# Performance work log

Hardware: AMD Instinct MI355X
Metric: run time of the kernel (lower is better)

## Reference

```python
import jax, jax.numpy as jnp
import numpy as np
from jax import lax

IMG_H, IMG_W = 800.0, 800.0
REG_WEIGHTS = (10.0, 10.0, 5.0, 5.0)
SCORE_THRESH = 0.05
NMS_THRESH = 0.5
NUM_DETECTIONS = 100
MIN_SIZE = 1.0
BBOX_XFORM_CLIP = float(np.log(1000.0 / 16.0))


def setup_inputs() -> dict:
    key = jax.random.key(0)
    k1, k2, k3, k4 = jax.random.split(key, 4)
    N, C = 1000, 81
    class_logit = jax.random.normal(k1, (N, C), dtype=jnp.float32) * 2.0
    box_regression = jax.random.normal(k2, (N, C * 4), dtype=jnp.float32)
    # proposals: valid (x1,y1,x2,y2) boxes inside the 800x800 image
    ctr = jax.random.uniform(k3, (N, 2), dtype=jnp.float32) * 800.0
    wh = jax.random.uniform(k4, (N, 2), dtype=jnp.float32) * 200.0 + 8.0
    x1y1 = jnp.clip(ctr - 0.5 * wh, 0.0, 800.0)
    x2y2 = jnp.clip(ctr + 0.5 * wh, 0.0, 800.0)
    proposal = jnp.concatenate([x1y1, x2y2], axis=1)
    return dict(class_logit=class_logit, box_regression=box_regression, proposal=proposal)


def decode_boxes(deltas, boxes):
    # deltas: [..., 4] (dx,dy,dw,dh); boxes: [..., 4] (x1,y1,x2,y2)
    wx, wy, ww, wh = REG_WEIGHTS
    widths = boxes[..., 2] - boxes[..., 0]
    heights = boxes[..., 3] - boxes[..., 1]
    ctr_x = boxes[..., 0] + 0.5 * widths
    ctr_y = boxes[..., 1] + 0.5 * heights
    dx = deltas[..., 0] / wx
    dy = deltas[..., 1] / wy
    dw = jnp.minimum(deltas[..., 2] / ww, BBOX_XFORM_CLIP)
    dh = jnp.minimum(deltas[..., 3] / wh, BBOX_XFORM_CLIP)
    pcx = dx * widths + ctr_x
    pcy = dy * heights + ctr_y
    pw = jnp.exp(dw) * widths
    ph = jnp.exp(dh) * heights
    return jnp.stack([pcx - 0.5 * pw, pcy - 0.5 * ph, pcx + 0.5 * pw, pcy + 0.5 * ph], axis=-1)


def pairwise_iou(b):
    # b: [N, 4] -> [N, N]
    area = (b[:, 2] - b[:, 0]) * (b[:, 3] - b[:, 1])
    lt = jnp.maximum(b[:, None, :2], b[None, :, :2])
    rb = jnp.minimum(b[:, None, 2:], b[None, :, 2:])
    wh = jnp.clip(rb - lt, 0.0)
    inter = wh[..., 0] * wh[..., 1]
    return inter / (area[:, None] + area[None, :] - inter + 1e-9)


def nms_one_class(boxes, scores):
    # boxes: [N, 4]; scores: [N] with invalid entries masked to -1.
    # Exact greedy NMS: sort by score desc, suppress IoU > NMS_THRESH.
    N = boxes.shape[0]
    order = jnp.argsort(-scores)
    b = boxes[order]
    s = scores[order]
    iou = pairwise_iou(b)
    valid = s > -0.5

    def body(carry, xs):
        keep, i = carry
        row, v = xs
        suppressed = jnp.any(keep & (row > NMS_THRESH))
        keep = keep.at[i].set(v & jnp.logical_not(suppressed))
        return (keep, i + 1), None

    (keep, _), _ = lax.scan(body, (jnp.zeros((N,), bool), jnp.int32(0)), (iou, valid))
    s_kept = jnp.where(keep, s, -1.0)
    top_s, top_i = lax.top_k(s_kept, NUM_DETECTIONS)  # kept are already score-sorted
    out_valid = top_s > -0.5
    out_boxes = jnp.where(out_valid[:, None], b[top_i], 0.0)
    out_scores = jnp.where(out_valid, top_s, 0.0)
    return out_boxes, out_scores, out_valid


def reference(class_logit, box_regression, proposal):
    N, C = class_logit.shape
    pred_score = jax.nn.softmax(class_logit, axis=-1)           # [N, C]
    deltas = box_regression.reshape(N, C, 4)
    boxes = decode_boxes(deltas[:, 1:, :], proposal[:, None, :])  # [N, C-1, 4]
    # clip to image (process_box)
    boxes = jnp.stack([
        jnp.clip(boxes[..., 0], 0.0, IMG_W),
        jnp.clip(boxes[..., 1], 0.0, IMG_H),
        jnp.clip(boxes[..., 2], 0.0, IMG_W),
        jnp.clip(boxes[..., 3], 0.0, IMG_H),
    ], axis=-1)
    w = boxes[..., 2] - boxes[..., 0]
    h = boxes[..., 3] - boxes[..., 1]
    score_fg = pred_score[:, 1:]                                 # [N, C-1]
    valid = (score_fg >= SCORE_THRESH) & (w >= MIN_SIZE) & (h >= MIN_SIZE)
    scores_m = jnp.where(valid, score_fg, -1.0)
    boxes_c = jnp.transpose(boxes, (1, 0, 2))                    # [C-1, N, 4]
    scores_c = scores_m.T                                        # [C-1, N]
    out_boxes, out_scores, out_valid = jax.vmap(nms_one_class)(boxes_c, scores_c)
    labels = jnp.broadcast_to(jnp.arange(1, C, dtype=jnp.int32)[:, None], out_scores.shape)
    labels = jnp.where(out_valid, labels, 0)
    # padded per-class detections: boxes [C-1, D, 4], scores/labels/valid [C-1, D]
    return out_boxes, out_scores, labels, out_valid
```

## Files before the change

### kernel.cpp

```cpp
#include <hip/hip_runtime.h>
#include <math.h>

#define N_PROP   1000
#define C_ALL    81
#define N_FG     80
#define TOPK     100
#define CAP      1024
#define IMG_WH   800.0f
#define SCORE_TH 0.05f
#define NMS_TH   0.5f
#define MIN_SZ   1.0f
#define BBOX_CLIP 4.135166556742356f

#define BLK      512

typedef unsigned long long u64;

__global__ __launch_bounds__(BLK) void roihead_kernel(
    const float* __restrict__ logits,
    const float* __restrict__ boxreg,
    const float* __restrict__ prop,
    float* __restrict__ out)
{
    __shared__ float2 s_stats[N_PROP];
    __shared__ u64   s_key[CAP];
    __shared__ float cx1[CAP], cy1[CAP], cx2[CAP], cy2[CAP], car[CAP];
    __shared__ u64   s_skey[CAP];
    __shared__ float sx1[CAP], sy1[CAP], sx2[CAP], sy2[CAP], sar[CAP];
    __shared__ u64   s_mask[256 * 4];
    __shared__ u64   s_keep[4];
    __shared__ unsigned char s_rem[CAP];
    __shared__ int   s_cnt, s_emit;

    const int c   = blockIdx.x;
    const int tid = threadIdx.x;
    const int col = c + 1;

    const int OFF_SCORES = N_FG * TOPK * 4;
    const int OFF_LABELS = OFF_SCORES + N_FG * TOPK;
    const int OFF_VALID  = OFF_LABELS + N_FG * TOPK;

    if (tid < 175) {
        float4 z = make_float4(0.f, 0.f, 0.f, 0.f);
        if (tid < 100)      ((float4*)(out + c * TOPK * 4))[tid] = z;
        else if (tid < 125) ((float4*)(out + OFF_SCORES + c * TOPK))[tid - 100] = z;
        else if (tid < 150) ((float4*)(out + OFF_LABELS + c * TOPK))[tid - 125] = z;
        else                ((float4*)(out + OFF_VALID  + c * TOPK))[tid - 150] = z;
    }
    if (tid == 0) { s_cnt = 0; s_emit = 0; }

    for (int n = tid; n < N_PROP; n += BLK) {
        const float* row = logits + n * C_ALL;
        float rv[C_ALL];
        #pragma unroll
        for (int j = 0; j < C_ALL; ++j) rv[j] = row[j];
        float m = rv[0];
        #pragma unroll
        for (int j = 1; j < C_ALL; ++j) m = fmaxf(m, rv[j]);
        float s = 0.0f;
        #pragma unroll
        for (int j = 0; j < C_ALL; ++j) s += expf(rv[j] - m);
        s_stats[n] = make_float2(m, s);
    }
    __syncthreads();

    for (int n = tid; n < N_PROP; n += BLK) {
        float2 ms = s_stats[n];
        float score = expf(logits[n * C_ALL + col] - ms.x) / ms.y;

        float4 p = *(const float4*)(prop + n * 4);
        float w  = p.z - p.x;
        float h  = p.w - p.y;
        float pcx0 = p.x + 0.5f * w;
        float pcy0 = p.y + 0.5f * h;

        float4 d = *(const float4*)(boxreg + n * (C_ALL * 4) + col * 4);
        float dx = d.x / 10.0f;
        float dy = d.y / 10.0f;
        float dw = fminf(d.z / 5.0f, BBOX_CLIP);
        float dh = fminf(d.w / 5.0f, BBOX_CLIP);

        float pcx = dx * w + pcx0;
        float pcy = dy * h + pcy0;
        float pw  = expf(dw) * w;
        float ph  = expf(dh) * h;

        float x1 = fminf(fmaxf(pcx - 0.5f * pw, 0.0f), IMG_WH);
        float y1 = fminf(fmaxf(pcy - 0.5f * ph, 0.0f), IMG_WH);
        float x2 = fminf(fmaxf(pcx + 0.5f * pw, 0.0f), IMG_WH);
        float y2 = fminf(fmaxf(pcy + 0.5f * ph, 0.0f), IMG_WH);

        float bw = x2 - x1;
        float bh = y2 - y1;
        if (score >= SCORE_TH && bw >= MIN_SZ && bh >= MIN_SZ) {
            int slot = atomicAdd(&s_cnt, 1);
            unsigned int fb = __float_as_uint(score);
            s_key[slot] = ((u64)fb << 20) | ((u64)(1023 - n) << 10) | (u64)slot;
            cx1[slot] = x1; cy1[slot] = y1; cx2[slot] = x2; cy2[slot] = y2;
            car[slot] = bw * bh;
        }
    }
    __syncthreads();

    const int V = s_cnt;
    if (V == 0) return;

    for (int t = tid; t < V; t += BLK) {
        u64 myk = s_key[t];
        int rank = 0;
        #pragma unroll 4
        for (int j = 0; j < V; ++j) rank += (s_key[j] > myk) ? 1 : 0;
        s_skey[rank] = myk;
        sx1[rank] = cx1[t]; sy1[rank] = cy1[t];
        sx2[rank] = cx2[t]; sy2[rank] = cy2[t];
        sar[rank] = car[t];
    }
    __syncthreads();

    if (V <= 64) {
        if (tid < 64) {
            const int lane = tid;
            bool act = lane < V;
            float bx1 = 0.f, by1 = 0.f, bx2 = 0.f, by2 = 0.f, bar = 0.f;
            if (act) {
                bx1 = sx1[lane]; by1 = sy1[lane];
                bx2 = sx2[lane]; by2 = sy2[lane];
                bar = sar[lane];
            }
            u64 myrow = 0;
            for (int i = 0; i < V; ++i) {
                float ix1 = __shfl(bx1, i, 64);
                float iy1 = __shfl(by1, i, 64);
                float ix2 = __shfl(bx2, i, 64);
                float iy2 = __shfl(by2, i, 64);
                float iar = __shfl(bar, i, 64);
                float lx = fmaxf(ix1, bx1);
                float ly = fmaxf(iy1, by1);
                float rx = fminf(ix2, bx2);
                float ry = fminf(iy2, by2);
                float iw = fmaxf(rx - lx, 0.0f);
                float ih = fmaxf(ry - ly, 0.0f);
                float inter = iw * ih;
                float iou = inter / (iar + bar - inter + 1e-9f);
                u64 bal = __ballot(act && (iou > NMS_TH));
                if (lane == i) {
                    u64 upper = (i == 63) ? 0ull : ~((1ull << (i + 1)) - 1ull);
                    myrow = bal & upper;
                }
            }
            u64 S = 0, K = 0;
            for (int i = 0; i < V; ++i) {
                if (!((S >> i) & 1ull)) {
                    K |= 1ull << i;
                    S |= __shfl(myrow, i, 64);
                }
            }
            if (act && ((K >> lane) & 1ull)) {
                int rank = __popcll(K & ((1ull << lane) - 1ull));
                float score = __uint_as_float((unsigned int)(s_skey[lane] >> 20));
                out[(c * TOPK + rank) * 4 + 0] = bx1;
                out[(c * TOPK + rank) * 4 + 1] = by1;
                out[(c * TOPK + rank) * 4 + 2] = bx2;
                out[(c * TOPK + rank) * 4 + 3] = by2;
                out[OFF_SCORES + c * TOPK + rank] = score;
                out[OFF_LABELS + c * TOPK + rank] = (float)col;
                out[OFF_VALID  + c * TOPK + rank] = 1.0f;
            }
        }
    } else if (V <= 256) {
        for (int i = tid; i < V; i += BLK) {
            float x1i = sx1[i], y1i = sy1[i], x2i = sx2[i], y2i = sy2[i];
            float ai  = sar[i];
            for (int w = 0; w < 4; ++w) {
                u64 mrow = 0;
                int j0 = w << 6;
                int j1 = min(V, j0 + 64);
                for (int j = max(j0, i + 1); j < j1; ++j) {
                    float lx = fmaxf(x1i, sx1[j]);
                    float ly = fmaxf(y1i, sy1[j]);
                    float rx = fminf(x2i, sx2[j]);
                    float ry = fminf(y2i, sy2[j]);
                    float iw = fmaxf(rx - lx, 0.0f);
                    float ih = fmaxf(ry - ly, 0.0f);
                    float inter = iw * ih;
                    float iou = inter / (ai + sar[j] - inter + 1e-9f);
                    if (iou > NMS_TH) mrow |= 1ull << (j - j0);
                }
                s_mask[(i << 2) + w] = mrow;
            }
        }
        __syncthreads();

        if (tid == 0) {
            u64 r0 = 0, r1 = 0, r2 = 0, r3 = 0;
            u64 k0 = 0, k1 = 0, k2 = 0, k3 = 0;
            int kept = 0;
            u64 p0 = s_mask[0], p1 = s_mask[1], p2 = s_mask[2], p3 = s_mask[3];
            u64 q0 = 0, q1 = 0, q2 = 0, q3 = 0;
            if (V > 1) {
                const u64* nr = &s_mask[4];
                q0 = nr[0]; q1 = nr[1]; q2 = nr[2]; q3 = nr[3];
            }
            for (int i = 0; i < V; ++i) {
                u64 t0 = 0, t1 = 0, t2 = 0, t3 = 0;
                if (i + 2 < V) {
                    const u64* nr = &s_mask[(i + 2) << 2];
                    t0 = nr[0]; t1 = nr[1]; t2 = nr[2]; t3 = nr[3];
                }
                int w = i >> 6;
                u64 bit = 1ull << (i & 63);
                u64 rw = (w == 0) ? r0 : (w == 1) ? r1 : (w == 2) ? r2 : r3;
                if (!(rw & bit)) {
                    if (w == 0) k0 |= bit; else if (w == 1) k1 |= bit;
                    else if (w == 2) k2 |= bit; else k3 |= bit;
                    if (++kept >= TOPK) break;
                    r0 |= p0; r1 |= p1; r2 |= p2; r3 |= p3;
                }
                p0 = q0; p1 = q1; p2 = q2; p3 = q3;
                q0 = t0; q1 = t1; q2 = t2; q3 = t3;
            }
            s_keep[0] = k0; s_keep[1] = k1; s_keep[2] = k2; s_keep[3] = k3;
        }
        __syncthreads();

        u64 kw0 = s_keep[0], kw1 = s_keep[1], kw2 = s_keep[2], kw3 = s_keep[3];
        for (int t = tid; t < V; t += BLK) {
            int w = t >> 6;
            u64 kw = (w == 0) ? kw0 : (w == 1) ? kw1 : (w == 2) ? kw2 : kw3;
            if (!((kw >> (t & 63)) & 1ull)) continue;
            int rank = 0;
            if (w > 0) rank += __popcll(kw0);
            if (w > 1) rank += __popcll(kw1);
            if (w > 2) rank += __popcll(kw2);
            rank += __popcll(kw & ((1ull << (t & 63)) - 1ull));
            if (rank < TOPK) {
                float score = __uint_as_float((unsigned int)(s_skey[t] >> 20));
                out[(c * TOPK + rank) * 4 + 0] = sx1[t];
                out[(c * TOPK + rank) * 4 + 1] = sy1[t];
                out[(c * TOPK + rank) * 4 + 2] = sx2[t];
                out[(c * TOPK + rank) * 4 + 3] = sy2[t];
                out[OFF_SCORES + c * TOPK + rank] = score;
                out[OFF_LABELS + c * TOPK + rank] = (float)col;
                out[OFF_VALID  + c * TOPK + rank] = 1.0f;
            }
        }
    } else {
        for (int t = tid; t < V; t += BLK) s_rem[t] = 0;
        __syncthreads();
        for (int i = 0; i < V; ++i) {
            if (s_rem[i]) continue;
            if (tid == 0) {
                int k = s_emit;
                if (k < TOPK) {
                    float score = __uint_as_float((unsigned int)(s_skey[i] >> 20));
                    out[(c * TOPK + k) * 4 + 0] = sx1[i];
                    out[(c * TOPK + k) * 4 + 1] = sy1[i];
                    out[(c * TOPK + k) * 4 + 2] = sx2[i];
                    out[(c * TOPK + k) * 4 + 3] = sy2[i];
                    out[OFF_SCORES + c * TOPK + k] = score;
                    out[OFF_LABELS + c * TOPK + k] = (float)col;
                    out[OFF_VALID  + c * TOPK + k] = 1.0f;
                }
                s_emit = k + 1;
            }
            float x1i = sx1[i], y1i = sy1[i], x2i = sx2[i], y2i = sy2[i];
            float ai  = sar[i];
            for (int jj = i + 1 + tid; jj < V; jj += BLK) {
                if (s_rem[jj]) continue;
                float lx = fmaxf(x1i, sx1[jj]);
                float ly = fmaxf(y1i, sy1[jj]);
                float rx = fminf(x2i, sx2[jj]);
                float ry = fminf(y2i, sy2[jj]);
                float iw = fmaxf(rx - lx, 0.0f);
                float ih = fmaxf(ry - ly, 0.0f);
                float inter = iw * ih;
                float iou = inter / (ai + sar[jj] - inter + 1e-9f);
                if (iou > NMS_TH) s_rem[jj] = 1;
            }
            __syncthreads();
            if (s_emit >= TOPK) break;
        }
    }
}

extern "C" void kernel_launch(void* const* d_in, const int* in_sizes, int n_in,
                              void* d_out, int out_size, void* d_ws, size_t ws_size,
                              hipStream_t stream) {
    const float* class_logit = (const float*)d_in[0];
    const float* box_reg     = (const float*)d_in[1];
    const float* proposal    = (const float*)d_in[2];
    float* out = (float*)d_out;

    roihead_kernel<<<N_FG, BLK, 0, stream>>>(class_logit, box_reg, proposal,
                                             out);
}
```

Before: 93.66 us.

## Split softmax/decode into a separate grid-wide kernel feeding a per-class NMS kernel

Softmax and box decoding move into their own kernel with 250 blocks. Each block handles 4 proposals and uses wave-level shuffle reductions, so the softmax is no longer recomputed redundantly by all 80 class blocks. Candidates are appended through global atomics into per-class workspace buckets, and a second 256-thread NMS kernel loads them and runs the existing sort and NMS paths. This costs an extra memset, two kernel launches and a global-memory round trip. The sort key also drops its slot bits. The old fused kernel is kept as a fallback when the workspace is too small.

Measured after the change: 84.96 us. 9.3% less time.

```diff
diff --git a/kernel.cpp b/kernel.cpp
--- a/kernel.cpp
+++ b/kernel.cpp
@@ -12,17 +12,110 @@
 #define MIN_SZ   1.0f
 #define BBOX_CLIP 4.135166556742356f
 
-#define BLK      512
+#define DEC_BLK  320
+#define NMS_BLK  256
 
 typedef unsigned long long u64;
 
-__global__ __launch_bounds__(BLK) void roihead_kernel(
+#define WS_CNT_STRIDE 16
+#define WS_KEYS_OFF   8192
+#define WS_FLT_OFF    (WS_KEYS_OFF + N_FG * CAP * 8)
+#define WS_REQUIRED   (WS_FLT_OFF + 5ull * N_FG * CAP * 4)
+
+__global__ __launch_bounds__(DEC_BLK) void decode_kernel(
     const float* __restrict__ logits,
     const float* __restrict__ boxreg,
     const float* __restrict__ prop,
+    char* __restrict__ ws)
+{
+    int*   cnt  = (int*)ws;
+    u64*   wkey = (u64*)(ws + WS_KEYS_OFF);
+    float* wx1  = (float*)(ws + WS_FLT_OFF);
+    float* wy1  = wx1 + N_FG * CAP;
+    float* wx2  = wy1 + N_FG * CAP;
+    float* wy2  = wx2 + N_FG * CAP;
+    float* war  = wy2 + N_FG * CAP;
+
+    __shared__ float2 s_ms[4];
+
+    const int b    = blockIdx.x;
+    const int tid  = threadIdx.x;
+    const int wave = tid >> 6;
+    const int lane = tid & 63;
+
+    if (wave < 4) {
+        const float* row = logits + (4 * b + wave) * C_ALL;
+        float v1 = row[lane];
+        float v2 = (lane < C_ALL - 64) ? row[64 + lane] : 0.f;
+
+        float m = (lane < C_ALL - 64) ? fmaxf(v1, v2) : v1;
+        #pragma unroll
+        for (int off = 32; off >= 1; off >>= 1)
+            m = fmaxf(m, __shfl_xor(m, off, 64));
+
+        float s = expf(v1 - m) + ((lane < C_ALL - 64) ? expf(v2 - m) : 0.0f);
+        #pragma unroll
+        for (int off = 32; off >= 1; off >>= 1)
+            s += __shfl_xor(s, off, 64);
+
+        if (lane == 0) s_ms[wave] = make_float2(m, s);
+    }
+    __syncthreads();
+
+    const int r   = tid / N_FG;
+    const int cc  = tid - r * N_FG;
+    const int n   = 4 * b + r;
+    const int col = cc + 1;
+
+    float2 ms = s_ms[r];
+    float score = expf(logits[n * C_ALL + col] - ms.x) / ms.y;
+
+    float4 p = *(const float4*)(prop + n * 4);
+    float w  = p.z - p.x;
+    float h  = p.w - p.y;
+    float pcx0 = p.x + 0.5f * w;
+    float pcy0 = p.y + 0.5f * h;
+
+    float4 d = *(const float4*)(boxreg + n * (C_ALL * 4) + col * 4);
+    float dx = d.x / 10.0f;
+    float dy = d.y / 10.0f;
+    float dw = fminf(d.z / 5.0f, BBOX_CLIP);
+    float dh = fminf(d.w / 5.0f, BBOX_CLIP);
+
+    float pcx = dx * w + pcx0;
+    float pcy = dy * h + pcy0;
+    float pw  = expf(dw) * w;
+    float ph  = expf(dh) * h;
+
+    float x1 = fminf(fmaxf(pcx - 0.5f * pw, 0.0f), IMG_WH);
+    float y1 = fminf(fmaxf(pcy - 0.5f * ph, 0.0f), IMG_WH);
+    float x2 = fminf(fmaxf(pcx + 0.5f * pw, 0.0f), IMG_WH);
+    float y2 = fminf(fmaxf(pcy + 0.5f * ph, 0.0f), IMG_WH);
+
+    float bw = x2 - x1;
+    float bh = y2 - y1;
+    if (score >= SCORE_TH && bw >= MIN_SZ && bh >= MIN_SZ) {
+        int slot = atomicAdd(&cnt[cc * WS_CNT_STRIDE], 1);
+        unsigned int fb = __float_as_uint(score);
+        int base = cc * CAP + slot;
+        wkey[base] = ((u64)fb << 10) | (u64)(1023 - n);
+        wx1[base] = x1; wy1[base] = y1; wx2[base] = x2; wy2[base] = y2;
+        war[base] = bw * bh;
+    }
+}
+
+__global__ __launch_bounds__(NMS_BLK) void nms_kernel(
+    const char* __restrict__ ws,
     float* __restrict__ out)
 {
-    __shared__ float2 s_stats[N_PROP];
+    const int*   cnt  = (const int*)ws;
+    const u64*   wkey = (const u64*)(ws + WS_KEYS_OFF);
+    const float* wx1  = (const float*)(ws + WS_FLT_OFF);
+    const float* wy1  = wx1 + N_FG * CAP;
+    const float* wx2  = wy1 + N_FG * CAP;
+    const float* wy2  = wx2 + N_FG * CAP;
+    const float* war  = wy2 + N_FG * CAP;
+
     __shared__ u64   s_key[CAP];
     __shared__ float cx1[CAP], cy1[CAP], cx2[CAP], cy2[CAP], car[CAP];
     __shared__ u64   s_skey[CAP];
@@ -30,7 +123,7 @@
     __shared__ u64   s_mask[256 * 4];
     __shared__ u64   s_keep[4];
     __shared__ unsigned char s_rem[CAP];
-    __shared__ int   s_cnt, s_emit;
+    __shared__ int   s_emit;
 
     const int c   = blockIdx.x;
     const int tid = threadIdx.x;
@@ -47,65 +140,21 @@
         else if (tid < 150) ((float4*)(out + OFF_LABELS + c * TOPK))[tid - 125] = z;
         else                ((float4*)(out + OFF_VALID  + c * TOPK))[tid - 150] = z;
     }
-    if (tid == 0) { s_cnt = 0; s_emit = 0; }
-
-    for (int n = tid; n < N_PROP; n += BLK) {
-        const float* row = logits + n * C_ALL;
-        float rv[C_ALL];
-        #pragma unroll
-        for (int j = 0; j < C_ALL; ++j) rv[j] = row[j];
-        float m = rv[0];
-        #pragma unroll
-        for (int j = 1; j < C_ALL; ++j) m = fmaxf(m, rv[j]);
-        float s = 0.0f;
-        #pragma unroll
-        for (int j = 0; j < C_ALL; ++j) s += expf(rv[j] - m);
-        s_stats[n] = make_float2(m, s);
+    if (tid == 0) s_emit = 0;
+
+    const int V = cnt[c * WS_CNT_STRIDE];
+    if (V == 0) return;
+
+    for (int t = tid; t < V; t += NMS_BLK) {
+        int base = c * CAP + t;
+        s_key[t] = wkey[base];
+        cx1[t] = wx1[base]; cy1[t] = wy1[base];
+        cx2[t] = wx2[base]; cy2[t] = wy2[base];
+        car[t] = war[base];
     }
     __syncthreads();
 
-    for (int n = tid; n < N_PROP; n += BLK) {
-        float2 ms = s_stats[n];
-        float score = expf(logits[n * C_ALL + col] - ms.x) / ms.y;
-
-        float4 p = *(const float4*)(prop + n * 4);
-        float w  = p.z - p.x;
-        float h  = p.w - p.y;
-        float pcx0 = p.x + 0.5f * w;
-        float pcy0 = p.y + 0.5f * h;
-
-        float4 d = *(const float4*)(boxreg + n * (C_ALL * 4) + col * 4);
-        float dx = d.x / 10.0f;
-        float dy = d.y / 10.0f;
-        float dw = fminf(d.z / 5.0f, BBOX_CLIP);
-        float dh = fminf(d.w / 5.0f, BBOX_CLIP);
-
-        float pcx = dx * w + pcx0;
-        float pcy = dy * h + pcy0;
-        float pw  = expf(dw) * w;
-        float ph  = expf(dh) * h;
-
-        float x1 = fminf(fmaxf(pcx - 0.5f * pw, 0.0f), IMG_WH);
-        float y1 = fminf(fmaxf(pcy - 0.5f * ph, 0.0f), IMG_WH);
-        float x2 = fminf(fmaxf(pcx + 0.5f * pw, 0.0f), IMG_WH);
-        float y2 = fminf(fmaxf(pcy + 0.5f * ph, 0.0f), IMG_WH);
-
-        float bw = x2 - x1;
-        float bh = y2 - y1;
-        if (score >= SCORE_TH && bw >= MIN_SZ && bh >= MIN_SZ) {
-            int slot = atomicAdd(&s_cnt, 1);
-            unsigned int fb = __float_as_uint(score);
-            s_key[slot] = ((u64)fb << 20) | ((u64)(1023 - n) << 10) | (u64)slot;
-            cx1[slot] = x1; cy1[slot] = y1; cx2[slot] = x2; cy2[slot] = y2;
-            car[slot] = bw * bh;
-        }
-    }
-    __syncthreads();
-
-    const int V = s_cnt;
-    if (V == 0) return;
-
-    for (int t = tid; t < V; t += BLK) {
+    for (int t = tid; t < V; t += NMS_BLK) {
         u64 myk = s_key[t];
         int rank = 0;
         #pragma unroll 4
@@ -157,7 +206,7 @@
             }
             if (act && ((K >> lane) & 1ull)) {
                 int rank = __popcll(K & ((1ull << lane) - 1ull));
-                float score = __uint_as_float((unsigned int)(s_skey[lane] >> 20));
+                float score = __uint_as_float((unsigned int)(s_skey[lane] >> 10));
                 out[(c * TOPK + rank) * 4 + 0] = bx1;
                 out[(c * TOPK + rank) * 4 + 1] = by1;
                 out[(c * TOPK + rank) * 4 + 2] = bx2;
@@ -168,7 +217,7 @@
             }
         }
     } else if (V <= 256) {
-        for (int i = tid; i < V; i += BLK) {
+        for (int i = tid; i < V; i += NMS_BLK) {
             float x1i = sx1[i], y1i = sy1[i], x2i = sx2[i], y2i = sy2[i];
             float ai  = sar[i];
             for (int w = 0; w < 4; ++w) {
@@ -224,7 +273,248 @@
         __syncthreads();
 
         u64 kw0 = s_keep[0], kw1 = s_keep[1], kw2 = s_keep[2], kw3 = s_keep[3];
-        for (int t = tid; t < V; t += BLK) {
+        for (int t = tid; t < V; t += NMS_BLK) {
+            int w = t >> 6;
+            u64 kw = (w == 0) ? kw0 : (w == 1) ? kw1 : (w == 2) ? kw2 : kw3;
+            if (!((kw >> (t & 63)) & 1ull)) continue;
+            int rank = 0;
+            if (w > 0) rank += __popcll(kw0);
+            if (w > 1) rank += __popcll(kw1);
+            if (w > 2) rank += __popcll(kw2);
+            rank += __popcll(kw & ((1ull << (t & 63)) - 1ull));
+            if (rank < TOPK) {
+                float score = __uint_as_float((unsigned int)(s_skey[t] >> 10));
+                out[(c * TOPK + rank) * 4 + 0] = sx1[t];
+                out[(c * TOPK + rank) * 4 + 1] = sy1[t];
+                out[(c * TOPK + rank) * 4 + 2] = sx2[t];
+                out[(c * TOPK + rank) * 4 + 3] = sy2[t];
+                out[OFF_SCORES + c * TOPK + rank] = score;
+                out[OFF_LABELS + c * TOPK + rank] = (float)col;
+                out[OFF_VALID  + c * TOPK + rank] = 1.0f;
+            }
+        }
+    } else {
+        for (int t = tid; t < V; t += NMS_BLK) s_rem[t] = 0;
+        __syncthreads();
+        for (int i = 0; i < V; ++i) {
+            if (s_rem[i]) continue;
+            if (tid == 0) {
+                int k = s_emit;
+                if (k < TOPK) {
+                    float score = __uint_as_float((unsigned int)(s_skey[i] >> 10));
+                    out[(c * TOPK + k) * 4 + 0] = sx1[i];
+                    out[(c * TOPK + k) * 4 + 1] = sy1[i];
+                    out[(c * TOPK + k) * 4 + 2] = sx2[i];
+                    out[(c * TOPK + k) * 4 + 3] = sy2[i];
+                    out[OFF_SCORES + c * TOPK + k] = score;
+                    out[OFF_LABELS + c * TOPK + k] = (float)col;
+                    out[OFF_VALID  + c * TOPK + k] = 1.0f;
+                }
+                s_emit = k + 1;
+            }
+            float x1i = sx1[i], y1i = sy1[i], x2i = sx2[i], y2i = sy2[i];
+            float ai  = sar[i];
+            for (int jj = i + 1 + tid; jj < V; jj += NMS_BLK) {
+                if (s_rem[jj]) continue;
+                float lx = fmaxf(x1i, sx1[jj]);
+                float ly = fmaxf(y1i, sy1[jj]);
+                float rx = fminf(x2i, sx2[jj]);
+                float ry = fminf(y2i, sy2[jj]);
+                float iw = fmaxf(rx - lx, 0.0f);
+                float ih = fmaxf(ry - ly, 0.0f);
+                float inter = iw * ih;
+                float iou = inter / (ai + sar[jj] - inter + 1e-9f);
+                if (iou > NMS_TH) s_rem[jj] = 1;
+            }
+            __syncthreads();
+            if (s_emit >= TOPK) break;
+        }
+    }
+}
+
+__global__ __launch_bounds__(512) void roihead_fused_kernel(
+    const float* __restrict__ logits,
+    const float* __restrict__ boxreg,
+    const float* __restrict__ prop,
+    float* __restrict__ out)
+{
+    __shared__ float2 s_stats[N_PROP];
+    __shared__ u64   s_key[CAP];
+    __shared__ float cx1[CAP], cy1[CAP], cx2[CAP], cy2[CAP], car[CAP];
+    __shared__ u64   s_skey[CAP];
+    __shared__ float sx1[CAP], sy1[CAP], sx2[CAP], sy2[CAP], sar[CAP];
+    __shared__ u64   s_mask[256 * 4];
+    __shared__ u64   s_keep[4];
+    __shared__ unsigned char s_rem[CAP];
+    __shared__ int   s_cnt, s_emit;
+
+    const int c   = blockIdx.x;
+    const int tid = threadIdx.x;
+    const int col = c + 1;
+
+    const int OFF_SCORES = N_FG * TOPK * 4;
+    const int OFF_LABELS = OFF_SCORES + N_FG * TOPK;
+    const int OFF_VALID  = OFF_LABELS + N_FG * TOPK;
+
+    if (tid < 175) {
+        float4 z = make_float4(0.f, 0.f, 0.f, 0.f);
+        if (tid < 100)      ((float4*)(out + c * TOPK * 4))[tid] = z;
+        else if (tid < 125) ((float4*)(out + OFF_SCORES + c * TOPK))[tid - 100] = z;
+        else if (tid < 150) ((float4*)(out + OFF_LABELS + c * TOPK))[tid - 125] = z;
+        else                ((float4*)(out + OFF_VALID  + c * TOPK))[tid - 150] = z;
+    }
+    if (tid == 0) { s_cnt = 0; s_emit = 0; }
+
+    for (int n = tid; n < N_PROP; n += 512) {
+        const float* row = logits + n * C_ALL;
+        float m = -1e30f;
+        for (int j = 0; j < C_ALL; ++j) m = fmaxf(m, row[j]);
+        float s = 0.0f;
+        for (int j = 0; j < C_ALL; ++j) s += expf(row[j] - m);
+        s_stats[n] = make_float2(m, s);
+    }
+    __syncthreads();
+
+    for (int n = tid; n < N_PROP; n += 512) {
+        float2 ms = s_stats[n];
+        float score = expf(logits[n * C_ALL + col] - ms.x) / ms.y;
+        float4 p = *(const float4*)(prop + n * 4);
+        float w  = p.z - p.x;
+        float h  = p.w - p.y;
+        float pcx0 = p.x + 0.5f * w;
+        float pcy0 = p.y + 0.5f * h;
+        float4 d = *(const float4*)(boxreg + n * (C_ALL * 4) + col * 4);
+        float dx = d.x / 10.0f;
+        float dy = d.y / 10.0f;
+        float dw = fminf(d.z / 5.0f, BBOX_CLIP);
+        float dh = fminf(d.w / 5.0f, BBOX_CLIP);
+        float pcx = dx * w + pcx0;
+        float pcy = dy * h + pcy0;
+        float pw  = expf(dw) * w;
+        float ph  = expf(dh) * h;
+        float x1 = fminf(fmaxf(pcx - 0.5f * pw, 0.0f), IMG_WH);
+        float y1 = fminf(fmaxf(pcy - 0.5f * ph, 0.0f), IMG_WH);
+        float x2 = fminf(fmaxf(pcx + 0.5f * pw, 0.0f), IMG_WH);
+        float y2 = fminf(fmaxf(pcy + 0.5f * ph, 0.0f), IMG_WH);
+        float bw = x2 - x1;
+        float bh = y2 - y1;
+        if (score >= SCORE_TH && bw >= MIN_SZ && bh >= MIN_SZ) {
+            int slot = atomicAdd(&s_cnt, 1);
+            unsigned int fb = __float_as_uint(score);
+            s_key[slot] = ((u64)fb << 20) | ((u64)(1023 - n) << 10) | (u64)slot;
+            cx1[slot] = x1; cy1[slot] = y1; cx2[slot] = x2; cy2[slot] = y2;
+            car[slot] = bw * bh;
+        }
+    }
+    __syncthreads();
+
+    const int V = s_cnt;
+    if (V == 0) return;
+
+    for (int t = tid; t < V; t += 512) {
+        u64 myk = s_key[t];
+        int rank = 0;
+        for (int j = 0; j < V; ++j) rank += (s_key[j] > myk) ? 1 : 0;
+        s_skey[rank] = myk;
+        sx1[rank] = cx1[t]; sy1[rank] = cy1[t];
+        sx2[rank] = cx2[t]; sy2[rank] = cy2[t];
+        sar[rank] = car[t];
+    }
+    __syncthreads();
+
+    if (V <= 64) {
+        if (tid < 64) {
+            const int lane = tid;
+            bool act = lane < V;
+            float bx1 = 0.f, by1 = 0.f, bx2 = 0.f, by2 = 0.f, bar = 0.f;
+            if (act) {
+                bx1 = sx1[lane]; by1 = sy1[lane];
+                bx2 = sx2[lane]; by2 = sy2[lane];
+                bar = sar[lane];
+            }
+            u64 myrow = 0;
+            for (int i = 0; i < V; ++i) {
+                float ix1 = __shfl(bx1, i, 64);
+                float iy1 = __shfl(by1, i, 64);
+                float ix2 = __shfl(bx2, i, 64);
+                float iy2 = __shfl(by2, i, 64);
+                float iar = __shfl(bar, i, 64);
+                float lx = fmaxf(ix1, bx1);
+                float ly = fmaxf(iy1, by1);
+                float rx = fminf(ix2, bx2);
+                float ry = fminf(iy2, by2);
+                float iw = fmaxf(rx - lx, 0.0f);
+                float ih = fmaxf(ry - ly, 0.0f);
+                float inter = iw * ih;
+                float iou = inter / (iar + bar - inter + 1e-9f);
+                u64 bal = __ballot(act && (iou > NMS_TH));
+                if (lane == i) {
+                    u64 upper = (i == 63) ? 0ull : ~((1ull << (i + 1)) - 1ull);
+                    myrow = bal & upper;
+                }
+            }
+            u64 S = 0, K = 0;
+            for (int i = 0; i < V; ++i) {
+                if (!((S >> i) & 1ull)) {
+                    K |= 1ull << i;
+                    S |= __shfl(myrow, i, 64);
+                }
+            }
+            if (act && ((K >> lane) & 1ull)) {
+                int rank = __popcll(K & ((1ull << lane) - 1ull));
+                float score = __uint_as_float((unsigned int)(s_skey[lane] >> 20));
+                out[(c * TOPK + rank) * 4 + 0] = bx1;
+                out[(c * TOPK + rank) * 4 + 1] = by1;
+                out[(c * TOPK + rank) * 4 + 2] = bx2;
+                out[(c * TOPK + rank) * 4 + 3] = by2;
+                out[OFF_SCORES + c * TOPK + rank] = score;
+                out[OFF_LABELS + c * TOPK + rank] = (float)col;
+                out[OFF_VALID  + c * TOPK + rank] = 1.0f;
+            }
+        }
+    } else if (V <= 256) {
+        for (int i = tid; i < V; i += 512) {
+            float x1i = sx1[i], y1i = sy1[i], x2i = sx2[i], y2i = sy2[i];
+            float ai  = sar[i];
+            for (int w = 0; w < 4; ++w) {
+                u64 mrow = 0;
+                int j0 = w << 6;
+                int j1 = min(V, j0 + 64);
+                for (int j = max(j0, i + 1); j < j1; ++j) {
+                    float lx = fmaxf(x1i, sx1[j]);
+                    float ly = fmaxf(y1i, sy1[j]);
+                    float rx = fminf(x2i, sx2[j]);
+                    float ry = fminf(y2i, sy2[j]);
+                    float iw = fmaxf(rx - lx, 0.0f);
+                    float ih = fmaxf(ry - ly, 0.0f);
+                    float inter = iw * ih;
+                    float iou = inter / (ai + sar[j] - inter + 1e-9f);
+                    if (iou > NMS_TH) mrow |= 1ull << (j - j0);
+                }
+                s_mask[(i << 2) + w] = mrow;
+            }
+        }
+        __syncthreads();
+        if (tid == 0) {
+            u64 r0 = 0, r1 = 0, r2 = 0, r3 = 0;
+            u64 k0 = 0, k1 = 0, k2 = 0, k3 = 0;
+            int kept = 0;
+            for (int i = 0; i < V; ++i) {
+                int w = i >> 6;
+                u64 bit = 1ull << (i & 63);
+                u64 rw = (w == 0) ? r0 : (w == 1) ? r1 : (w == 2) ? r2 : r3;
+                if (rw & bit) continue;
+                if (w == 0) k0 |= bit; else if (w == 1) k1 |= bit;
+                else if (w == 2) k2 |= bit; else k3 |= bit;
+                if (++kept >= TOPK) break;
+                const u64* mr = &s_mask[i << 2];
+                r0 |= mr[0]; r1 |= mr[1]; r2 |= mr[2]; r3 |= mr[3];
+            }
+            s_keep[0] = k0; s_keep[1] = k1; s_keep[2] = k2; s_keep[3] = k3;
+        }
+        __syncthreads();
+        u64 kw0 = s_keep[0], kw1 = s_keep[1], kw2 = s_keep[2], kw3 = s_keep[3];
+        for (int t = tid; t < V; t += 512) {
             int w = t >> 6;
             u64 kw = (w == 0) ? kw0 : (w == 1) ? kw1 : (w == 2) ? kw2 : kw3;
             if (!((kw >> (t & 63)) & 1ull)) continue;
@@ -245,7 +535,7 @@
             }
         }
     } else {
-        for (int t = tid; t < V; t += BLK) s_rem[t] = 0;
+        for (int t = tid; t < V; t += 512) s_rem[t] = 0;
         __syncthreads();
         for (int i = 0; i < V; ++i) {
             if (s_rem[i]) continue;
@@ -265,7 +555,7 @@
             }
             float x1i = sx1[i], y1i = sy1[i], x2i = sx2[i], y2i = sy2[i];
             float ai  = sar[i];
-            for (int jj = i + 1 + tid; jj < V; jj += BLK) {
+            for (int jj = i + 1 + tid; jj < V; jj += 512) {
                 if (s_rem[jj]) continue;
                 float lx = fmaxf(x1i, sx1[jj]);
                 float ly = fmaxf(y1i, sy1[jj]);
@@ -291,6 +581,13 @@
     const float* proposal    = (const float*)d_in[2];
     float* out = (float*)d_out;
 
-    roihead_kernel<<<N_FG, BLK, 0, stream>>>(class_logit, box_reg, proposal,
-                                             out);
+    if (ws_size >= WS_REQUIRED) {
+        hipMemsetAsync(d_ws, 0, N_FG * WS_CNT_STRIDE * sizeof(int), stream);
+        decode_kernel<<<N_PROP / 4, DEC_BLK, 0, stream>>>(
+            class_logit, box_reg, proposal, (char*)d_ws);
+        nms_kernel<<<N_FG, NMS_BLK, 0, stream>>>((const char*)d_ws, out);
+    } else {
+        roihead_fused_kernel<<<N_FG, 512, 0, stream>>>(
+            class_logit, box_reg, proposal, out);
+    }
 }
```

## Split softmax stats into separate kernel and prefilter candidates by score before decode

Applied to the files above, without the earlier changes.

Softmax max/sum stats are computed once by a new wave-per-row kernel into workspace, instead of redundantly in each of the 80 class blocks. Each class block then uses ballot compaction to keep only proposals passing the score threshold and decodes boxes only for those. Output writes are deferred to a single pass over a kept-index list, replacing the separate zero-fill and per-branch scatter writes. Block size drops to 256, and the sort key is shortened. The cost is an extra kernel launch and a dependency on the workspace being large enough, with a slow fallback path otherwise.

New measurement: 83.62 us. -10.7%, faster.

```diff
diff --git a/kernel.cpp b/kernel.cpp
--- a/kernel.cpp
+++ b/kernel.cpp
@@ -12,61 +12,106 @@
 #define MIN_SZ   1.0f
 #define BBOX_CLIP 4.135166556742356f
 
-#define BLK      512
-
 typedef unsigned long long u64;
 
-__global__ __launch_bounds__(BLK) void roihead_kernel(
+#define WS_REQUIRED (sizeof(float2) * N_PROP)
+
+__global__ __launch_bounds__(256) void stats_kernel(
+    const float* __restrict__ logits,
+    float2* __restrict__ stats)
+{
+    const int wave = threadIdx.x >> 6;
+    const int lane = threadIdx.x & 63;
+    const int n = blockIdx.x * 4 + wave;
+    if (n >= N_PROP) return;
+    const float* row = logits + n * C_ALL;
+
+    float v1 = row[lane];
+    float v2 = (lane < C_ALL - 64) ? row[64 + lane] : 0.f;
+
+    float m = (lane < C_ALL - 64) ? fmaxf(v1, v2) : v1;
+    #pragma unroll
+    for (int off = 32; off >= 1; off >>= 1)
+        m = fmaxf(m, __shfl_xor(m, off, 64));
+
+    float s = expf(v1 - m) + ((lane < C_ALL - 64) ? expf(v2 - m) : 0.0f);
+    #pragma unroll
+    for (int off = 32; off >= 1; off >>= 1)
+        s += __shfl_xor(s, off, 64);
+
+    if (lane == 0) stats[n] = make_float2(m, s);
+}
+
+__global__ __launch_bounds__(256) void nms_kernel(
     const float* __restrict__ logits,
     const float* __restrict__ boxreg,
     const float* __restrict__ prop,
+    const float2* __restrict__ stats,
     float* __restrict__ out)
 {
-    __shared__ float2 s_stats[N_PROP];
+    __shared__ float2 s_ms[N_PROP];
+    __shared__ unsigned short s_cn[CAP];
+    __shared__ float s_csc[CAP];
     __shared__ u64   s_key[CAP];
     __shared__ float cx1[CAP], cy1[CAP], cx2[CAP], cy2[CAP], car[CAP];
     __shared__ u64   s_skey[CAP];
     __shared__ float sx1[CAP], sy1[CAP], sx2[CAP], sy2[CAP], sar[CAP];
     __shared__ u64   s_mask[256 * 4];
-    __shared__ u64   s_keep[4];
     __shared__ unsigned char s_rem[CAP];
-    __shared__ int   s_cnt, s_emit;
-
-    const int c   = blockIdx.x;
-    const int tid = threadIdx.x;
-    const int col = c + 1;
+    __shared__ unsigned short s_src[TOPK];
+    __shared__ int   s_nc, s_cnt, s_emit, s_nk;
+
+    const int c    = blockIdx.x;
+    const int tid  = threadIdx.x;
+    const int lane = tid & 63;
+    const int col  = c + 1;
 
     const int OFF_SCORES = N_FG * TOPK * 4;
     const int OFF_LABELS = OFF_SCORES + N_FG * TOPK;
     const int OFF_VALID  = OFF_LABELS + N_FG * TOPK;
 
-    if (tid < 175) {
-        float4 z = make_float4(0.f, 0.f, 0.f, 0.f);
-        if (tid < 100)      ((float4*)(out + c * TOPK * 4))[tid] = z;
-        else if (tid < 125) ((float4*)(out + OFF_SCORES + c * TOPK))[tid - 100] = z;
-        else if (tid < 150) ((float4*)(out + OFF_LABELS + c * TOPK))[tid - 125] = z;
-        else                ((float4*)(out + OFF_VALID  + c * TOPK))[tid - 150] = z;
-    }
-    if (tid == 0) { s_cnt = 0; s_emit = 0; }
-
-    for (int n = tid; n < N_PROP; n += BLK) {
-        const float* row = logits + n * C_ALL;
-        float rv[C_ALL];
-        #pragma unroll
-        for (int j = 0; j < C_ALL; ++j) rv[j] = row[j];
-        float m = rv[0];
-        #pragma unroll
-        for (int j = 1; j < C_ALL; ++j) m = fmaxf(m, rv[j]);
-        float s = 0.0f;
-        #pragma unroll
-        for (int j = 0; j < C_ALL; ++j) s += expf(rv[j] - m);
-        s_stats[n] = make_float2(m, s);
+    if (tid == 0) { s_nc = 0; s_cnt = 0; s_emit = 0; s_nk = 0; }
+
+    if (stats != nullptr) {
+        for (int t = tid; t < N_PROP; t += 256) s_ms[t] = stats[t];
+    } else {
+        for (int n = tid; n < N_PROP; n += 256) {
+            const float* row = logits + n * C_ALL;
+            float m = -1e30f;
+            for (int j = 0; j < C_ALL; ++j) m = fmaxf(m, row[j]);
+            float s = 0.0f;
+            for (int j = 0; j < C_ALL; ++j) s += expf(row[j] - m);
+            s_ms[n] = make_float2(m, s);
+        }
     }
     __syncthreads();
 
-    for (int n = tid; n < N_PROP; n += BLK) {
-        float2 ms = s_stats[n];
-        float score = expf(logits[n * C_ALL + col] - ms.x) / ms.y;
+    #pragma unroll
+    for (int k = 0; k < 4; ++k) {
+        int n = k * 256 + tid;
+        bool v = false; float sc = 0.0f;
+        if (n < N_PROP) {
+            float2 ms = s_ms[n];
+            sc = expf(logits[n * C_ALL + col] - ms.x) / ms.y;
+            v = (sc >= SCORE_TH);
+        }
+        u64 bal = __ballot(v);
+        int pop = __popcll(bal);
+        int wb = 0;
+        if (lane == 0 && pop) wb = atomicAdd(&s_nc, pop);
+        wb = __shfl(wb, 0, 64);
+        if (v) {
+            int slot = wb + __popcll(bal & ((1ull << lane) - 1ull));
+            s_cn[slot]  = (unsigned short)n;
+            s_csc[slot] = sc;
+        }
+    }
+    __syncthreads();
+    const int NC = s_nc;
+
+    for (int t = tid; t < NC; t += 256) {
+        int n = s_cn[t];
+        float sc = s_csc[t];
 
         float4 p = *(const float4*)(prop + n * 4);
         float w  = p.z - p.x;
@@ -92,10 +137,9 @@
 
         float bw = x2 - x1;
         float bh = y2 - y1;
-        if (score >= SCORE_TH && bw >= MIN_SZ && bh >= MIN_SZ) {
+        if (bw >= MIN_SZ && bh >= MIN_SZ) {
             int slot = atomicAdd(&s_cnt, 1);
-            unsigned int fb = __float_as_uint(score);
-            s_key[slot] = ((u64)fb << 20) | ((u64)(1023 - n) << 10) | (u64)slot;
+            s_key[slot] = ((u64)__float_as_uint(sc) << 10) | (u64)(1023 - n);
             cx1[slot] = x1; cy1[slot] = y1; cx2[slot] = x2; cy2[slot] = y2;
             car[slot] = bw * bh;
         }
@@ -103,183 +147,162 @@
     __syncthreads();
 
     const int V = s_cnt;
-    if (V == 0) return;
-
-    for (int t = tid; t < V; t += BLK) {
-        u64 myk = s_key[t];
-        int rank = 0;
-        #pragma unroll 4
-        for (int j = 0; j < V; ++j) rank += (s_key[j] > myk) ? 1 : 0;
-        s_skey[rank] = myk;
-        sx1[rank] = cx1[t]; sy1[rank] = cy1[t];
-        sx2[rank] = cx2[t]; sy2[rank] = cy2[t];
-        sar[rank] = car[t];
-    }
-    __syncthreads();
-
-    if (V <= 64) {
-        if (tid < 64) {
-            const int lane = tid;
-            bool act = lane < V;
-            float bx1 = 0.f, by1 = 0.f, bx2 = 0.f, by2 = 0.f, bar = 0.f;
-            if (act) {
-                bx1 = sx1[lane]; by1 = sy1[lane];
-                bx2 = sx2[lane]; by2 = sy2[lane];
-                bar = sar[lane];
-            }
-            u64 myrow = 0;
-            for (int i = 0; i < V; ++i) {
-                float ix1 = __shfl(bx1, i, 64);
-                float iy1 = __shfl(by1, i, 64);
-                float ix2 = __shfl(bx2, i, 64);
-                float iy2 = __shfl(by2, i, 64);
-                float iar = __shfl(bar, i, 64);
-                float lx = fmaxf(ix1, bx1);
-                float ly = fmaxf(iy1, by1);
-                float rx = fminf(ix2, bx2);
-                float ry = fminf(iy2, by2);
-                float iw = fmaxf(rx - lx, 0.0f);
-                float ih = fmaxf(ry - ly, 0.0f);
-                float inter = iw * ih;
-                float iou = inter / (iar + bar - inter + 1e-9f);
-                u64 bal = __ballot(act && (iou > NMS_TH));
-                if (lane == i) {
-                    u64 upper = (i == 63) ? 0ull : ~((1ull << (i + 1)) - 1ull);
-                    myrow = bal & upper;
-                }
-            }
-            u64 S = 0, K = 0;
-            for (int i = 0; i < V; ++i) {
-                if (!((S >> i) & 1ull)) {
-                    K |= 1ull << i;
-                    S |= __shfl(myrow, i, 64);
-                }
-            }
-            if (act && ((K >> lane) & 1ull)) {
-                int rank = __popcll(K & ((1ull << lane) - 1ull));
-                float score = __uint_as_float((unsigned int)(s_skey[lane] >> 20));
-                out[(c * TOPK + rank) * 4 + 0] = bx1;
-                out[(c * TOPK + rank) * 4 + 1] = by1;
-                out[(c * TOPK + rank) * 4 + 2] = bx2;
-                out[(c * TOPK + rank) * 4 + 3] = by2;
-                out[OFF_SCORES + c * TOPK + rank] = score;
-                out[OFF_LABELS + c * TOPK + rank] = (float)col;
-                out[OFF_VALID  + c * TOPK + rank] = 1.0f;
-            }
-        }
-    } else if (V <= 256) {
-        for (int i = tid; i < V; i += BLK) {
-            float x1i = sx1[i], y1i = sy1[i], x2i = sx2[i], y2i = sy2[i];
-            float ai  = sar[i];
-            for (int w = 0; w < 4; ++w) {
-                u64 mrow = 0;
-                int j0 = w << 6;
-                int j1 = min(V, j0 + 64);
-                for (int j = max(j0, i + 1); j < j1; ++j) {
-                    float lx = fmaxf(x1i, sx1[j]);
-                    float ly = fmaxf(y1i, sy1[j]);
-                    float rx = fminf(x2i, sx2[j]);
-                    float ry = fminf(y2i, sy2[j]);
+
+    if (V > 0) {
+        for (int t = tid; t < V; t += 256) {
+            u64 myk = s_key[t];
+            int rank = 0;
+            #pragma unroll 4
+            for (int j = 0; j < V; ++j) rank += (s_key[j] > myk) ? 1 : 0;
+            s_skey[rank] = myk;
+            sx1[rank] = cx1[t]; sy1[rank] = cy1[t];
+            sx2[rank] = cx2[t]; sy2[rank] = cy2[t];
+            sar[rank] = car[t];
+        }
+        __syncthreads();
+
+        if (V <= 64) {
+            if (tid < 64) {
+                bool act = lane < V;
+                float bx1 = 0.f, by1 = 0.f, bx2 = 0.f, by2 = 0.f, bar = 0.f;
+                if (act) {
+                    bx1 = sx1[lane]; by1 = sy1[lane];
+                    bx2 = sx2[lane]; by2 = sy2[lane];
+                    bar = sar[lane];
+                }
+                u64 myrow = 0;
+                for (int i = 0; i < V; ++i) {
+                    float ix1 = __shfl(bx1, i, 64);
+                    float iy1 = __shfl(by1, i, 64);
+                    float ix2 = __shfl(bx2, i, 64);
+                    float iy2 = __shfl(by2, i, 64);
+                    float iar = __shfl(bar, i, 64);
+                    float lx = fmaxf(ix1, bx1);
+                    float ly = fmaxf(iy1, by1);
+                    float rx = fminf(ix2, bx2);
+                    float ry = fminf(iy2, by2);
                     float iw = fmaxf(rx - lx, 0.0f);
                     float ih = fmaxf(ry - ly, 0.0f);
                     float inter = iw * ih;
-                    float iou = inter / (ai + sar[j] - inter + 1e-9f);
-                    if (iou > NMS_TH) mrow |= 1ull << (j - j0);
-                }
-                s_mask[(i << 2) + w] = mrow;
+                    float iou = inter / (iar + bar - inter + 1e-9f);
+                    u64 bal = __ballot(act && (iou > NMS_TH));
+                    if (lane == i) {
+                        u64 upper = (i == 63) ? 0ull : ~((1ull << (i + 1)) - 1ull);
+                        myrow = bal & upper;
+                    }
+                }
+                u64 S = 0, K = 0;
+                for (int i = 0; i < V; ++i) {
+                    if (!((S >> i) & 1ull)) {
+                        K |= 1ull << i;
+                        S |= __shfl(myrow, i, 64);
+                    }
+                }
+                if (act && ((K >> lane) & 1ull)) {
+                    int rank = __popcll(K & ((1ull << lane) - 1ull));
+                    s_src[rank] = (unsigned short)lane;
+                }
+                if (lane == 0) s_nk = __popcll(K);
             }
-        }
-        __syncthreads();
-
-        if (tid == 0) {
-            u64 r0 = 0, r1 = 0, r2 = 0, r3 = 0;
-            u64 k0 = 0, k1 = 0, k2 = 0, k3 = 0;
-            int kept = 0;
-            u64 p0 = s_mask[0], p1 = s_mask[1], p2 = s_mask[2], p3 = s_mask[3];
-            u64 q0 = 0, q1 = 0, q2 = 0, q3 = 0;
-            if (V > 1) {
-                const u64* nr = &s_mask[4];
-                q0 = nr[0]; q1 = nr[1]; q2 = nr[2]; q3 = nr[3];
-            }
-            for (int i = 0; i < V; ++i) {
-                u64 t0 = 0, t1 = 0, t2 = 0, t3 = 0;
-                if (i + 2 < V) {
-                    const u64* nr = &s_mask[(i + 2) << 2];
-                    t0 = nr[0]; t1 = nr[1]; t2 = nr[2]; t3 = nr[3];
-                }
-                int w = i >> 6;
-                u64 bit = 1ull << (i & 63);
-                u64 rw = (w == 0) ? r0 : (w == 1) ? r1 : (w == 2) ? r2 : r3;
-                if (!(rw & bit)) {
-                    if (w == 0) k0 |= bit; else if (w == 1) k1 |= bit;
-                    else if (w == 2) k2 |= bit; else k3 |= bit;
-                    if (++kept >= TOPK) break;
-                    r0 |= p0; r1 |= p1; r2 |= p2; r3 |= p3;
-                }
-                p0 = q0; p1 = q1; p2 = q2; p3 = q3;
-                q0 = t0; q1 = t1; q2 = t2; q3 = t3;
-            }
-            s_keep[0] = k0; s_keep[1] = k1; s_keep[2] = k2; s_keep[3] = k3;
-        }
-        __syncthreads();
-
-        u64 kw0 = s_keep[0], kw1 = s_keep[1], kw2 = s_keep[2], kw3 = s_keep[3];
-        for (int t = tid; t < V; t += BLK) {
-            int w = t >> 6;
-            u64 kw = (w == 0) ? kw0 : (w == 1) ? kw1 : (w == 2) ? kw2 : kw3;
-            if (!((kw >> (t & 63)) & 1ull)) continue;
-            int rank = 0;
-            if (w > 0) rank += __popcll(kw0);
-            if (w > 1) rank += __popcll(kw1);
-            if (w > 2) rank += __popcll(kw2);
-            rank += __popcll(kw & ((1ull << (t & 63)) - 1ull));
-            if (rank < TOPK) {
-                float score = __uint_as_float((unsigned int)(s_skey[t] >> 20));
-                out[(c * TOPK + rank) * 4 + 0] = sx1[t];
-                out[(c * TOPK + rank) * 4 + 1] = sy1[t];
-                out[(c * TOPK + rank) * 4 + 2] = sx2[t];
-                out[(c * TOPK + rank) * 4 + 3] = sy2[t];
-                out[OFF_SCORES + c * TOPK + rank] = score;
-                out[OFF_LABELS + c * TOPK + rank] = (float)col;
-                out[OFF_VALID  + c * TOPK + rank] = 1.0f;
-            }
-        }
-    } else {
-        for (int t = tid; t < V; t += BLK) s_rem[t] = 0;
-        __syncthreads();
-        for (int i = 0; i < V; ++i) {
-            if (s_rem[i]) continue;
-            if (tid == 0) {
-                int k = s_emit;
-                if (k < TOPK) {
-                    float score = __uint_as_float((unsigned int)(s_skey[i] >> 20));
-                    out[(c * TOPK + k) * 4 + 0] = sx1[i];
-                    out[(c * TOPK + k) * 4 + 1] = sy1[i];
-                    out[(c * TOPK + k) * 4 + 2] = sx2[i];
-                    out[(c * TOPK + k) * 4 + 3] = sy2[i];
-                    out[OFF_SCORES + c * TOPK + k] = score;
-                    out[OFF_LABELS + c * TOPK + k] = (float)col;
-                    out[OFF_VALID  + c * TOPK + k] = 1.0f;
-                }
-                s_emit = k + 1;
-            }
-            float x1i = sx1[i], y1i = sy1[i], x2i = sx2[i], y2i = sy2[i];
-            float ai  = sar[i];
-            for (int jj = i + 1 + tid; jj < V; jj += BLK) {
-                if (s_rem[jj]) continue;
-                float lx = fmaxf(x1i, sx1[jj]);
-                float ly = fmaxf(y1i, sy1[jj]);
-                float rx = fminf(x2i, sx2[jj]);
-                float ry = fminf(y2i, sy2[jj]);
-                float iw = fmaxf(rx - lx, 0.0f);
-                float ih = fmaxf(ry - ly, 0.0f);
-                float inter = iw * ih;
-                float iou = inter / (ai + sar[jj] - inter + 1e-9f);
-                if (iou > NMS_TH) s_rem[jj] = 1;
+        } else if (V <= 256) {
+            for (int i = tid; i < V; i += 256) {
+                float x1i = sx1[i], y1i = sy1[i], x2i = sx2[i], y2i = sy2[i];
+                float ai  = sar[i];
+                for (int w = 0; w < 4; ++w) {
+                    u64 mrow = 0;
+                    int j0 = w << 6;
+                    int j1 = min(V, j0 + 64);
+                    for (int j = max(j0, i + 1); j < j1; ++j) {
+                        float lx = fmaxf(x1i, sx1[j]);
+                        float ly = fmaxf(y1i, sy1[j]);
+                        float rx = fminf(x2i, sx2[j]);
+                        float ry = fminf(y2i, sy2[j]);
+                        float iw = fmaxf(rx - lx, 0.0f);
+                        float ih = fmaxf(ry - ly, 0.0f);
+                        float inter = iw * ih;
+                        float iou = inter / (ai + sar[j] - inter + 1e-9f);
+                        if (iou > NMS_TH) mrow |= 1ull << (j - j0);
+                    }
+                    s_mask[(i << 2) + w] = mrow;
+                }
             }
             __syncthreads();
-            if (s_emit >= TOPK) break;
-        }
+
+            if (tid == 0) {
+                u64 r0 = 0, r1 = 0, r2 = 0, r3 = 0;
+                int kept = 0;
+                u64 p0 = s_mask[0], p1 = s_mask[1], p2 = s_mask[2], p3 = s_mask[3];
+                u64 q0 = 0, q1 = 0, q2 = 0, q3 = 0;
+                if (V > 1) {
+                    const u64* nr = &s_mask[4];
+                    q0 = nr[0]; q1 = nr[1]; q2 = nr[2]; q3 = nr[3];
+                }
+                for (int i = 0; i < V; ++i) {
+                    u64 t0 = 0, t1 = 0, t2 = 0, t3 = 0;
+                    if (i + 2 < V) {
+                        const u64* nr = &s_mask[(i + 2) << 2];
+                        t0 = nr[0]; t1 = nr[1]; t2 = nr[2]; t3 = nr[3];
+                    }
+                    int w = i >> 6;
+                    u64 bit = 1ull << (i & 63);
+                    u64 rw = (w == 0) ? r0 : (w == 1) ? r1 : (w == 2) ? r2 : r3;
+                    if (!(rw & bit)) {
+                        s_src[kept] = (unsigned short)i;
+                        if (++kept >= TOPK) break;
+                        r0 |= p0; r1 |= p1; r2 |= p2; r3 |= p3;
+                    }
+                    p0 = q0; p1 = q1; p2 = q2; p3 = q3;
+                    q0 = t0; q1 = t1; q2 = t2; q3 = t3;
+                }
+                s_nk = kept;
+            }
+        } else {
+            for (int t = tid; t < V; t += 256) s_rem[t] = 0;
+            __syncthreads();
+            for (int i = 0; i < V; ++i) {
+                if (s_rem[i]) continue;
+                if (tid == 0) {
+                    int k = s_emit;
+                    if (k < TOPK) s_src[k] = (unsigned short)i;
+                    s_emit = k + 1;
+                }
+                float x1i = sx1[i], y1i = sy1[i], x2i = sx2[i], y2i = sy2[i];
+                float ai  = sar[i];
+                for (int jj = i + 1 + tid; jj < V; jj += 256) {
+                    if (s_rem[jj]) continue;
+                    float lx = fmaxf(x1i, sx1[jj]);
+                    float ly = fmaxf(y1i, sy1[jj]);
+                    float rx = fminf(x2i, sx2[jj]);
+                    float ry = fminf(y2i, sy2[jj]);
+                    float iw = fmaxf(rx - lx, 0.0f);
+                    float ih = fmaxf(ry - ly, 0.0f);
+                    float inter = iw * ih;
+                    float iou = inter / (ai + sar[jj] - inter + 1e-9f);
+                    if (iou > NMS_TH) s_rem[jj] = 1;
+                }
+                __syncthreads();
+                if (s_emit >= TOPK) break;
+            }
+            if (tid == 0) s_nk = min(s_emit, TOPK);
+        }
+    }
+    __syncthreads();
+
+    const int nk = s_nk;
+    if (tid < TOPK) {
+        float4 bx = make_float4(0.f, 0.f, 0.f, 0.f);
+        float sc = 0.f, lb = 0.f, vd = 0.f;
+        if (tid < nk) {
+            int s = s_src[tid];
+            bx = make_float4(sx1[s], sy1[s], sx2[s], sy2[s]);
+            sc = __uint_as_float((unsigned int)(s_skey[s] >> 10));
+            lb = (float)col;
+            vd = 1.0f;
+        }
+        ((float4*)out)[c * TOPK + tid] = bx;
+        out[OFF_SCORES + c * TOPK + tid] = sc;
+        out[OFF_LABELS + c * TOPK + tid] = lb;
+        out[OFF_VALID  + c * TOPK + tid] = vd;
     }
 }
 
@@ -291,6 +314,11 @@
     const float* proposal    = (const float*)d_in[2];
     float* out = (float*)d_out;
 
-    roihead_kernel<<<N_FG, BLK, 0, stream>>>(class_logit, box_reg, proposal,
-                                             out);
+    float2* stats = (ws_size >= WS_REQUIRED) ? (float2*)d_ws : nullptr;
+
+    if (stats) {
+        stats_kernel<<<(N_PROP + 3) / 4, 256, 0, stream>>>(class_logit, stats);
+    }
+    nms_kernel<<<N_FG, 256, 0, stream>>>(class_logit, box_reg, proposal,
+                                         stats, out);
 }
```
